# Performance work log

Measured on AMD Instinct MI355X. Metric: run time of the kernel, lower is better.

Reference implementation:

```python
import jax, jax.numpy as jnp
import numpy as np

N_NODES = 50000
LN_EPS = 1e-5


def gcn_conv(x, src, dst, norm, W, b):
    # PyG GCNConv: h = x @ W, then symmetric-normalized scatter-add, then bias.
    h = x @ W                                   # [N, out]
    msg = h[src] * norm[:, None]                # [E+N, out] gathered, scaled
    out = jax.ops.segment_sum(msg, dst, num_segments=N_NODES)
    return out + b


def layer_norm(x, gamma, beta):
    mu = jnp.mean(x, axis=-1, keepdims=True)
    var = jnp.var(x, axis=-1, keepdims=True)
    return (x - mu) * jax.lax.rsqrt(var + LN_EPS) * gamma + beta


def setup_inputs() -> dict:
    key = jax.random.key(0)
    ks = jax.random.split(key, 8)
    N, E, D = N_NODES, 1600000, 128
    x = jax.random.normal(ks[0], (N, D), dtype=jnp.float32)
    edge_index = jax.random.randint(ks[1], (2, E), 0, N, dtype=jnp.int64)
    s = 1.0 / np.sqrt(D)
    return {
        "x": x,
        "edge_index": edge_index,
        "W1": jax.random.uniform(ks[2], (D, D), jnp.float32, -s, s),
        "b1": jnp.zeros((D,), jnp.float32),
        "g1": jnp.ones((D,), jnp.float32),
        "be1": jnp.zeros((D,), jnp.float32),
        "W2": jax.random.uniform(ks[3], (D, D), jnp.float32, -s, s),
        "b2": jnp.zeros((D,), jnp.float32),
        "g2": jnp.ones((D,), jnp.float32),
        "be2": jnp.zeros((D,), jnp.float32),
    }


def reference(x, edge_index, W1, b1, g1, be1, W2, b2, g2, be2):
    # Add self-loops (PyG GCNConv default add_self_loops=True)
    sl = jnp.arange(N_NODES, dtype=edge_index.dtype)
    src = jnp.concatenate([edge_index[0], sl])
    dst = jnp.concatenate([edge_index[1], sl])
    # Symmetric normalization: deg^{-1/2}[src] * deg^{-1/2}[dst]
    deg = jax.ops.segment_sum(jnp.ones_like(src, dtype=x.dtype), dst,
                              num_segments=N_NODES)
    dinv = jnp.where(deg > 0, jax.lax.rsqrt(deg), 0.0)
    norm = dinv[src] * dinv[dst]

    h = gcn_conv(x, src, dst, norm, W1, b1)
    h = jax.nn.elu(layer_norm(h, g1, be1))
    h = gcn_conv(h, src, dst, norm, W2, b2)
    h = jax.nn.elu(layer_norm(h, g2, be2))
    return h
```

## Files before the change

### kernel.cpp

```cpp
#include <hip/hip_runtime.h>
#include <hip/hip_bf16.h>
#include <math.h>

#define N_NODES 50000
#define D 128
#define LN_EPS 1e-5f
#define NB 391
#define CHUNK 4096
#define GB 782
#define HB 512

typedef unsigned int u32;
typedef unsigned short u16;
typedef __attribute__((ext_vector_type(8))) short bf16x8;
typedef __attribute__((ext_vector_type(8))) unsigned short u16x8;
typedef __attribute__((ext_vector_type(4))) float f32x4;

static __device__ __forceinline__ u16 f2bf(float f) {
    union { float f; unsigned u; } v; v.f = f;
    unsigned r = v.u + 0x7fff + ((v.u >> 16) & 1);
    return (u16)(r >> 16);
}
static __device__ __forceinline__ float bf2f(u16 b) {
    union { unsigned u; float f; } v; v.u = ((unsigned)b) << 16;
    return v.f;
}
static __device__ __forceinline__ bf16x8 packf8(const float* p) {
    float4 f0 = *(const float4*)p;
    float4 f1 = *(const float4*)(p + 4);
    bf16x8 r;
    r[0] = (short)f2bf(f0.x); r[1] = (short)f2bf(f0.y);
    r[2] = (short)f2bf(f0.z); r[3] = (short)f2bf(f0.w);
    r[4] = (short)f2bf(f1.x); r[5] = (short)f2bf(f1.y);
    r[6] = (short)f2bf(f1.z); r[7] = (short)f2bf(f1.w);
    return r;
}

static __device__ __forceinline__ void agg_core8(
        const u16* __restrict__ H, const u16* __restrict__ csr_src,
        const float* __restrict__ dinv, int s, int cnt, int c0, float dn,
        float* __restrict__ a) {
    float b[8];
#pragma unroll
    for (int i = 0; i < 8; ++i) { a[i] = 0.f; b[i] = 0.f; }
    const u16* cp = csr_src + s;
    int j = 0;
    for (; j + 8 <= cnt; j += 8) {
        u32 i0 = cp[j],     i1 = cp[j + 1], i2 = cp[j + 2], i3 = cp[j + 3];
        u32 i4 = cp[j + 4], i5 = cp[j + 5], i6 = cp[j + 6], i7 = cp[j + 7];
        u16x8 g0 = *(const u16x8*)&H[(size_t)i0 * D + c0];
        u16x8 g1 = *(const u16x8*)&H[(size_t)i1 * D + c0];
        u16x8 g2 = *(const u16x8*)&H[(size_t)i2 * D + c0];
        u16x8 g3 = *(const u16x8*)&H[(size_t)i3 * D + c0];
        u16x8 g4 = *(const u16x8*)&H[(size_t)i4 * D + c0];
        u16x8 g5 = *(const u16x8*)&H[(size_t)i5 * D + c0];
        u16x8 g6 = *(const u16x8*)&H[(size_t)i6 * D + c0];
        u16x8 g7 = *(const u16x8*)&H[(size_t)i7 * D + c0];
        float w0 = dinv[i0] * dn, w1 = dinv[i1] * dn;
        float w2 = dinv[i2] * dn, w3 = dinv[i3] * dn;
        float w4 = dinv[i4] * dn, w5 = dinv[i5] * dn;
        float w6 = dinv[i6] * dn, w7 = dinv[i7] * dn;
#pragma unroll
        for (int i = 0; i < 8; ++i) {
            a[i] = fmaf(w0, bf2f(g0[i]), a[i]);
            b[i] = fmaf(w1, bf2f(g1[i]), b[i]);
            a[i] = fmaf(w2, bf2f(g2[i]), a[i]);
            b[i] = fmaf(w3, bf2f(g3[i]), b[i]);
            a[i] = fmaf(w4, bf2f(g4[i]), a[i]);
            b[i] = fmaf(w5, bf2f(g5[i]), b[i]);
            a[i] = fmaf(w6, bf2f(g6[i]), a[i]);
            b[i] = fmaf(w7, bf2f(g7[i]), b[i]);
        }
    }
    for (; j < cnt; ++j) {
        u32 i0 = cp[j];
        u16x8 g0 = *(const u16x8*)&H[(size_t)i0 * D + c0];
        float w0 = dinv[i0] * dn;
#pragma unroll
        for (int i = 0; i < 8; ++i) a[i] = fmaf(w0, bf2f(g0[i]), a[i]);
    }
#pragma unroll
    for (int i = 0; i < 8; ++i) a[i] += b[i];
}

static __device__ __forceinline__ void ln_elu8(
        float* __restrict__ a, int c0,
        const float* __restrict__ bias, const float* __restrict__ gamma,
        const float* __restrict__ beta) {
    float4 bv0 = *(const float4*)&bias[c0];
    float4 bv1 = *(const float4*)&bias[c0 + 4];
    a[0] += bv0.x; a[1] += bv0.y; a[2] += bv0.z; a[3] += bv0.w;
    a[4] += bv1.x; a[5] += bv1.y; a[6] += bv1.z; a[7] += bv1.w;
    float sum = 0.f, sq = 0.f;
#pragma unroll
    for (int i = 0; i < 8; ++i) { sum += a[i]; sq = fmaf(a[i], a[i], sq); }
#pragma unroll
    for (int m = 8; m > 0; m >>= 1) {
        sum += __shfl_xor(sum, m, 64);
        sq  += __shfl_xor(sq,  m, 64);
    }
    float mean = sum * (1.f / 128.f);
    float var  = sq * (1.f / 128.f) - mean * mean;
    float rstd = rsqrtf(var + LN_EPS);
    float4 gv0 = *(const float4*)&gamma[c0];
    float4 gv1 = *(const float4*)&gamma[c0 + 4];
    float4 ev0 = *(const float4*)&beta[c0];
    float4 ev1 = *(const float4*)&beta[c0 + 4];
    float gg[8] = {gv0.x, gv0.y, gv0.z, gv0.w, gv1.x, gv1.y, gv1.z, gv1.w};
    float ee[8] = {ev0.x, ev0.y, ev0.z, ev0.w, ev1.x, ev1.y, ev1.z, ev1.w};
#pragma unroll
    for (int i = 0; i < 8; ++i) {
        float y = (a[i] - mean) * rstd * gg[i] + ee[i];
        a[i] = y > 0.f ? y : expm1f(y);
    }
}

__global__ __launch_bounds__(256) void transpose_w(const float* __restrict__ W1,
                                                   const float* __restrict__ W2,
                                                   u16* __restrict__ W1T,
                                                   u16* __restrict__ W2T) {
    const float* w = (blockIdx.x == 0) ? W1 : W2;
    u16* wt = (blockIdx.x == 0) ? W1T : W2T;
    for (int idx = threadIdx.x; idx < D * D; idx += 256)
        wt[(idx & 127) * D + (idx >> 7)] = f2bf(w[idx]);
}

__global__ __launch_bounds__(256) void gemm1_hist(const float* __restrict__ X,
                                                  const u16* __restrict__ W1T,
                                                  u16* __restrict__ H,
                                                  const int* __restrict__ dstA,
                                                  u32* __restrict__ bucketCount, int E) {
    __shared__ u32 hist[NB];

    if (blockIdx.x >= GB) {
        for (int b = threadIdx.x; b < NB; b += 256) hist[b] = 0;
        __syncthreads();
        int stride = HB * 256;
        for (int e = (blockIdx.x - GB) * 256 + threadIdx.x; e < E; e += stride)
            atomicAdd(&hist[((u32)dstA[e]) >> 7], 1u);
        __syncthreads();
        for (int b = threadIdx.x; b < NB; b += 256)
            if (hist[b]) atomicAdd(&bucketCount[b], hist[b]);
        return;
    }
    int lane = threadIdx.x & 63;
    int wid  = threadIdx.x >> 6;
    int r    = lane & 15;
    int kg   = lane >> 4;

    for (int rb = blockIdx.x * 4 + wid; rb < N_NODES / 16; rb += GB * 4) {
        int row0 = rb * 16;
        const float* xp = X + (size_t)(row0 + r) * D + kg * 8;
        bf16x8 a0 = packf8(xp);      bf16x8 a1 = packf8(xp + 32);
        bf16x8 a2 = packf8(xp + 64); bf16x8 a3 = packf8(xp + 96);
#pragma unroll
        for (int tile = 0; tile < 8; ++tile) {
            const u16* wp = W1T + (size_t)(tile * 16 + r) * D + kg * 8;
            f32x4 acc = {0.f, 0.f, 0.f, 0.f};
            acc = __builtin_amdgcn_mfma_f32_16x16x32_bf16(a0, *(const bf16x8*)(wp),      acc, 0, 0, 0);
            acc = __builtin_amdgcn_mfma_f32_16x16x32_bf16(a1, *(const bf16x8*)(wp + 32), acc, 0, 0, 0);
            acc = __builtin_amdgcn_mfma_f32_16x16x32_bf16(a2, *(const bf16x8*)(wp + 64), acc, 0, 0, 0);
            acc = __builtin_amdgcn_mfma_f32_16x16x32_bf16(a3, *(const bf16x8*)(wp + 96), acc, 0, 0, 0);
#pragma unroll
            for (int i = 0; i < 4; ++i)
                H[(size_t)(row0 + kg * 4 + i) * D + tile * 16 + r] = f2bf(acc[i]);
        }
    }
}

__global__ __launch_bounds__(512) void partition_kernel(const int* __restrict__ srcA,
                                                        const int* __restrict__ dstA,
                                                        const u32* __restrict__ bucketCount,
                                                        u32* __restrict__ relCursor,
                                                        u32* __restrict__ ebuf, int E) {
    __shared__ u32 sc[512];
    __shared__ u32 ebS[NB], cntA[NB], cntB[NB], base[NB];
    int t = threadIdx.x;
    u32 bc = (t < NB) ? bucketCount[t] : 0u;
    sc[t] = bc;
    for (int b = t; b < NB; b += 512) { cntA[b] = 0; cntB[b] = 0; }
    __syncthreads();
    for (int off = 1; off < 512; off <<= 1) {
        u32 v = sc[t] + ((t >= off) ? sc[t - off] : 0u);
        __syncthreads();
        sc[t] = v;
        __syncthreads();
    }
    if (t < NB) ebS[t] = sc[t] - bc;
    __syncthreads();

    int e0 = blockIdx.x * CHUNK;
    int e1 = min(e0 + CHUNK, E);
    for (int e = e0 + t; e < e1; e += 512)
        atomicAdd(&cntA[((u32)dstA[e]) >> 7], 1u);
    __syncthreads();
    for (int b = t; b < NB; b += 512)
        if (cntA[b]) base[b] = ebS[b] + atomicAdd(&relCursor[b], cntA[b]);
    __syncthreads();
    for (int e = e0 + t; e < e1; e += 512) {
        u32 d = (u32)dstA[e], sv = (u32)srcA[e];
        u32 b = d >> 7;
        u32 off = atomicAdd(&cntB[b], 1u);
        ebuf[base[b] + off] = (sv << 16) | d;
    }
}

__global__ __launch_bounds__(256) void bucket_build(const u32* __restrict__ ebuf,
                                                    const u32* __restrict__ bucketCount,
                                                    u16* __restrict__ csr_src,
                                                    int* __restrict__ startArr,
                                                    float* __restrict__ dinv) {
    int b = blockIdx.x, t = threadIdx.x;
    __shared__ u32 red[256];
    __shared__ u32 cnt[128], sc[128], cur[128];
    u32 partial = 0;
    for (int i = t; i < b; i += 256) partial += bucketCount[i];
    red[t] = partial;
    if (t < 128) cnt[t] = 0;
    __syncthreads();
    for (int off = 128; off > 0; off >>= 1) {
        if (t < off) red[t] += red[t + off];
        __syncthreads();
    }
    u32 eb0 = red[0];
    u32 eb1 = eb0 + bucketCount[b];
    u32 cs  = eb0 + 128u * (u32)b;

    int nodeBase = b << 7;
    int nNodes = min(128, N_NODES - nodeBase);
    for (u32 e = eb0 + t; e < eb1; e += 256)
        atomicAdd(&cnt[ebuf[e] & 127u], 1u);
    __syncthreads();
    u32 myCnt = 0;
    if (t < 128) {
        myCnt = (t < nNodes) ? cnt[t] + 1u : 0u;
        sc[t] = myCnt;
    }
    __syncthreads();
    for (int off = 1; off < 128; off <<= 1) {
        u32 v = 0;
        if (t < 128) v = sc[t] + ((t >= off) ? sc[t - off] : 0u);
        __syncthreads();
        if (t < 128) sc[t] = v;
        __syncthreads();
    }
    if (t < nNodes) {
        u32 excl = sc[t] - myCnt;
        int i = nodeBase + t;
        startArr[i] = (int)(cs + excl);
        dinv[i] = rsqrtf((float)myCnt);
        csr_src[cs + excl] = (u16)i;
        cur[t] = excl + 1u;
        if (b == NB - 1 && t == nNodes - 1)
            startArr[N_NODES] = (int)(cs + sc[t]);
    }
    __syncthreads();
    for (u32 e = eb0 + t; e < eb1; e += 256) {
        u32 p = ebuf[e];
        u32 pos = atomicAdd(&cur[p & 127u], 1u);
        csr_src[cs + pos] = (u16)(p >> 16);
    }
}

__global__ __launch_bounds__(256) void agg_gemm(
        const u16* __restrict__ H, const u16* __restrict__ csr_src,
        const int* __restrict__ startArr, const float* __restrict__ dinv,
        const float* __restrict__ bias, const float* __restrict__ gamma,
        const float* __restrict__ beta,
        const u16* __restrict__ W2T, u16* __restrict__ H2) {
    __shared__ __align__(16) u16 X2[16][136];

    int t = threadIdx.x;
    int grp = t >> 4;
    int l   = t & 15;
    int c0  = l * 8;
    int node = blockIdx.x * 16 + grp;
    int s   = startArr[node];
    int cnt = startArr[node + 1] - s;
    float dn = dinv[node];

    float a[8];
    agg_core8(H, csr_src, dinv, s, cnt, c0, dn, a);
    ln_elu8(a, c0, bias, gamma, beta);

    u16x8 o;
#pragma unroll
    for (int i = 0; i < 8; ++i) o[i] = f2bf(a[i]);
    *(u16x8*)&X2[grp][c0] = o;
    __syncthreads();

    int lane = t & 63;
    int wv   = t >> 6;
    int r    = lane & 15;
    int kg   = lane >> 4;
    int row0 = blockIdx.x * 16;

    const u16* xp = &X2[r][kg * 8];
    bf16x8 a0f = *(const bf16x8*)(xp);
    bf16x8 a1f = *(const bf16x8*)(xp + 32);
    bf16x8 a2f = *(const bf16x8*)(xp + 64);
    bf16x8 a3f = *(const bf16x8*)(xp + 96);
#pragma unroll
    for (int tile = wv; tile < 8; tile += 4) {
        const u16* wp = W2T + (size_t)(tile * 16 + r) * D + kg * 8;
        f32x4 acc = {0.f, 0.f, 0.f, 0.f};
        acc = __builtin_amdgcn_mfma_f32_16x16x32_bf16(a0f, *(const bf16x8*)(wp),      acc, 0, 0, 0);
        acc = __builtin_amdgcn_mfma_f32_16x16x32_bf16(a1f, *(const bf16x8*)(wp + 32), acc, 0, 0, 0);
        acc = __builtin_amdgcn_mfma_f32_16x16x32_bf16(a2f, *(const bf16x8*)(wp + 64), acc, 0, 0, 0);
        acc = __builtin_amdgcn_mfma_f32_16x16x32_bf16(a3f, *(const bf16x8*)(wp + 96), acc, 0, 0, 0);
#pragma unroll
        for (int i = 0; i < 4; ++i)
            H2[(size_t)(row0 + kg * 4 + i) * D + tile * 16 + r] = f2bf(acc[i]);
    }
}

__global__ __launch_bounds__(256) void agg_ln_elu(
        const u16* __restrict__ H, const u16* __restrict__ csr_src,
        const int* __restrict__ startArr, const float* __restrict__ dinv,
        const float* __restrict__ bias, const float* __restrict__ gamma,
        const float* __restrict__ beta, float* __restrict__ out) {
    int t = threadIdx.x;
    int node = blockIdx.x * 16 + (t >> 4);
    int l    = t & 15;
    int c0   = l * 8;
    int s    = startArr[node];
    int cnt  = startArr[node + 1] - s;
    float dn = dinv[node];

    float a[8];
    agg_core8(H, csr_src, dinv, s, cnt, c0, dn, a);
    ln_elu8(a, c0, bias, gamma, beta);

    f32x4 o0 = {a[0], a[1], a[2], a[3]};
    f32x4 o1 = {a[4], a[5], a[6], a[7]};
    float* op = out + (size_t)node * D + c0;
    __builtin_nontemporal_store(o0, (f32x4*)op);
    __builtin_nontemporal_store(o1, (f32x4*)(op + 4));
}

extern "C" void kernel_launch(void* const* d_in, const int* in_sizes, int n_in,
                              void* d_out, int out_size, void* d_ws, size_t ws_size,
                              hipStream_t stream) {
    const float* x   = (const float*)d_in[0];
    const int*  eidx = (const int*)d_in[1];
    const float* W1  = (const float*)d_in[2];
    const float* b1  = (const float*)d_in[3];
    const float* g1  = (const float*)d_in[4];
    const float* be1 = (const float*)d_in[5];
    const float* W2  = (const float*)d_in[6];
    const float* b2  = (const float*)d_in[7];
    const float* g2  = (const float*)d_in[8];
    const float* be2 = (const float*)d_in[9];

    int E = in_sizes[1] / 2;
    const int* srcA = eidx;
    const int* dstA = eidx + E;

    char* p = (char*)d_ws;
    auto alloc = [&](size_t bytes) {
        char* r = p;
        p += (bytes + 255) & ~(size_t)255;
        return r;
    };
    u32*   ctr      = (u32*)alloc((size_t)1024 * 4);
    u32*   ebuf     = (u32*)alloc((size_t)E * 4);
    u16*   csr_src  = (u16*)alloc((size_t)(E + N_NODES) * 2);
    int*   startArr = (int*)alloc((size_t)(N_NODES + 1) * 4);
    float* dinv     = (float*)alloc((size_t)N_NODES * 4);
    u16*   w1t      = (u16*)alloc((size_t)D * D * 2);
    u16*   w2t      = (u16*)alloc((size_t)D * D * 2);
    u16*   h        = (u16*)alloc((size_t)N_NODES * D * 2);
    u16*   h2       = (u16*)alloc((size_t)N_NODES * D * 2);
    float* outp     = (float*)d_out;

    u32* bucketCount = ctr;
    u32* relCursor   = ctr + 512;

    int pb = (E + CHUNK - 1) / CHUNK;
    int fb = N_NODES / 16;

    hipError_t e0 = hipMemsetAsync(ctr, 0, 1024 * 4, stream);
    (void)e0;
    transpose_w     <<<2, 256, 0, stream>>>(W1, W2, w1t, w2t);
    gemm1_hist      <<<GB + HB, 256, 0, stream>>>(x, w1t, h, dstA, bucketCount, E);
    partition_kernel<<<pb, 512, 0, stream>>>(srcA, dstA, bucketCount, relCursor, ebuf, E);
    bucket_build    <<<NB, 256, 0, stream>>>(ebuf, bucketCount, csr_src, startArr, dinv);
    agg_gemm        <<<fb, 256, 0, stream>>>(h, csr_src, startArr, dinv,
                                             b1, g1, be1, w2t, h2);
    agg_ln_elu      <<<fb, 256, 0, stream>>>(h2, csr_src, startArr, dinv,
                                             b2, g2, be2, outp);
}
```

Baseline: 295.1 us.

## Regroup kernels: fuse weight transpose with histogram, GEMM1 with partition

The weight transpose now runs as a tiled shared-memory transpose in 32 blocks beside the edge histogram, replacing the separate two-block transpose launch. The first GEMM moves out of the histogram kernel into the partition kernel, where extra blocks compute it alongside partitioning. This removes one launch and lets the serial two-block transpose run in parallel with the histogram. GEMM1 now runs with 512-thread blocks (8 waves per block), which may change occupancy and contend with partition work.

```diff
diff --git a/kernel.cpp b/kernel.cpp
--- a/kernel.cpp
+++ b/kernel.cpp
@@ -7,8 +7,10 @@
 #define LN_EPS 1e-5f
 #define NB 391
 #define CHUNK 4096
-#define GB 782
+#define TB 32
 #define HB 512
+#define PB 391
+#define GB2 391
 
 typedef unsigned int u32;
 typedef unsigned short u16;
@@ -115,40 +117,66 @@
     }
 }
 
-__global__ __launch_bounds__(256) void transpose_w(const float* __restrict__ W1,
-                                                   const float* __restrict__ W2,
-                                                   u16* __restrict__ W1T,
-                                                   u16* __restrict__ W2T) {
-    const float* w = (blockIdx.x == 0) ? W1 : W2;
-    u16* wt = (blockIdx.x == 0) ? W1T : W2T;
-    for (int idx = threadIdx.x; idx < D * D; idx += 256)
-        wt[(idx & 127) * D + (idx >> 7)] = f2bf(w[idx]);
-}
-
-__global__ __launch_bounds__(256) void gemm1_hist(const float* __restrict__ X,
-                                                  const u16* __restrict__ W1T,
-                                                  u16* __restrict__ H,
+__global__ __launch_bounds__(256) void trans_hist(const float* __restrict__ W1,
+                                                  const float* __restrict__ W2,
+                                                  u16* __restrict__ W1T,
+                                                  u16* __restrict__ W2T,
                                                   const int* __restrict__ dstA,
                                                   u32* __restrict__ bucketCount, int E) {
     __shared__ u32 hist[NB];
 
-    if (blockIdx.x >= GB) {
-        for (int b = threadIdx.x; b < NB; b += 256) hist[b] = 0;
-        __syncthreads();
-        int stride = HB * 256;
-        for (int e = (blockIdx.x - GB) * 256 + threadIdx.x; e < E; e += stride)
-            atomicAdd(&hist[((u32)dstA[e]) >> 7], 1u);
-        __syncthreads();
-        for (int b = threadIdx.x; b < NB; b += 256)
-            if (hist[b]) atomicAdd(&bucketCount[b], hist[b]);
+    if (blockIdx.x < TB) {
+        __shared__ u16 tile[32][33];
+        int mat  = blockIdx.x >> 4;
+        int tl   = blockIdx.x & 15;
+        int bi   = (tl >> 2) * 32;
+        int bj   = (tl & 3) * 32;
+        const float* w = mat ? W2 : W1;
+        u16* wt = mat ? W2T : W1T;
+        int t = threadIdx.x;
+        int lr = t >> 5, lc = t & 31;
+#pragma unroll
+        for (int pass = 0; pass < 4; ++pass) {
+            int r = lr + pass * 8;
+            tile[r][lc] = f2bf(w[(size_t)(bi + r) * D + bj + lc]);
+        }
+        __syncthreads();
+#pragma unroll
+        for (int pass = 0; pass < 4; ++pass) {
+            int c = lr + pass * 8;
+            wt[(size_t)(bj + c) * D + bi + lc] = tile[lc][c];
+        }
         return;
     }
-    int lane = threadIdx.x & 63;
-    int wid  = threadIdx.x >> 6;
-    int r    = lane & 15;
-    int kg   = lane >> 4;
-
-    for (int rb = blockIdx.x * 4 + wid; rb < N_NODES / 16; rb += GB * 4) {
+    for (int b = threadIdx.x; b < NB; b += 256) hist[b] = 0;
+    __syncthreads();
+    int stride = HB * 256;
+    for (int e = (blockIdx.x - TB) * 256 + threadIdx.x; e < E; e += stride)
+        atomicAdd(&hist[((u32)dstA[e]) >> 7], 1u);
+    __syncthreads();
+    for (int b = threadIdx.x; b < NB; b += 256)
+        if (hist[b]) atomicAdd(&bucketCount[b], hist[b]);
+}
+
+__global__ __launch_bounds__(512) void part_gemm(const int* __restrict__ srcA,
+                                                 const int* __restrict__ dstA,
+                                                 const u32* __restrict__ bucketCount,
+                                                 u32* __restrict__ relCursor,
+                                                 u32* __restrict__ ebuf, int E,
+                                                 const float* __restrict__ X,
+                                                 const u16* __restrict__ W1T,
+                                                 u16* __restrict__ H) {
+    __shared__ u32 sc[512];
+    __shared__ u32 ebS[NB], cntA[NB], cntB[NB], base[NB];
+    int t = threadIdx.x;
+
+    if (blockIdx.x >= PB) {
+        int lane = t & 63;
+        int wid  = t >> 6;
+        int r    = lane & 15;
+        int kg   = lane >> 4;
+        int rb   = (blockIdx.x - PB) * 8 + wid;
+        if (rb >= N_NODES / 16) return;
         int row0 = rb * 16;
         const float* xp = X + (size_t)(row0 + r) * D + kg * 8;
         bf16x8 a0 = packf8(xp);      bf16x8 a1 = packf8(xp + 32);
@@ -165,17 +193,9 @@
             for (int i = 0; i < 4; ++i)
                 H[(size_t)(row0 + kg * 4 + i) * D + tile * 16 + r] = f2bf(acc[i]);
         }
-    }
-}
-
-__global__ __launch_bounds__(512) void partition_kernel(const int* __restrict__ srcA,
-                                                        const int* __restrict__ dstA,
-                                                        const u32* __restrict__ bucketCount,
-                                                        u32* __restrict__ relCursor,
-                                                        u32* __restrict__ ebuf, int E) {
-    __shared__ u32 sc[512];
-    __shared__ u32 ebS[NB], cntA[NB], cntB[NB], base[NB];
-    int t = threadIdx.x;
+        return;
+    }
+
     u32 bc = (t < NB) ? bucketCount[t] : 0u;
     sc[t] = bc;
     for (int b = t; b < NB; b += 512) { cntA[b] = 0; cntB[b] = 0; }
@@ -376,17 +396,16 @@
     u32* bucketCount = ctr;
     u32* relCursor   = ctr + 512;
 
-    int pb = (E + CHUNK - 1) / CHUNK;
     int fb = N_NODES / 16;
 
     hipError_t e0 = hipMemsetAsync(ctr, 0, 1024 * 4, stream);
     (void)e0;
-    transpose_w     <<<2, 256, 0, stream>>>(W1, W2, w1t, w2t);
-    gemm1_hist      <<<GB + HB, 256, 0, stream>>>(x, w1t, h, dstA, bucketCount, E);
-    partition_kernel<<<pb, 512, 0, stream>>>(srcA, dstA, bucketCount, relCursor, ebuf, E);
-    bucket_build    <<<NB, 256, 0, stream>>>(ebuf, bucketCount, csr_src, startArr, dinv);
-    agg_gemm        <<<fb, 256, 0, stream>>>(h, csr_src, startArr, dinv,
-                                             b1, g1, be1, w2t, h2);
-    agg_ln_elu      <<<fb, 256, 0, stream>>>(h2, csr_src, startArr, dinv,
-                                             b2, g2, be2, outp);
-}
+    trans_hist  <<<TB + HB, 256, 0, stream>>>(W1, W2, w1t, w2t, dstA, bucketCount, E);
+    part_gemm   <<<PB + GB2, 512, 0, stream>>>(srcA, dstA, bucketCount, relCursor,
+                                               ebuf, E, x, w1t, h);
+    bucket_build<<<NB, 256, 0, stream>>>(ebuf, bucketCount, csr_src, startArr, dinv);
+    agg_gemm    <<<fb, 256, 0, stream>>>(h, csr_src, startArr, dinv,
+                                         b1, g1, be1, w2t, h2);
+    agg_ln_elu  <<<fb, 256, 0, stream>>>(h2, csr_src, startArr, dinv,
+                                         b2, g2, be2, outp);
+}
```

Result: faster. 278.9 us (-5.5%).

## Fuse weight transpose into gemm1_hist and stage W1 in shared memory

Applied to the files above, without the earlier changes.

Removes the separate two-block transpose_w launch. Each GEMM block now converts and transposes W1 into a padded LDS tile, and 16 extra blocks transpose W2 with a 32x32 shared tile. This removes one serial kernel launch and the slow two-block transpose, and the GEMM reads B fragments from LDS instead of global memory. In exchange, each of the 782 GEMM blocks redoes the 16K-element W1 conversion, uses about 35KB of LDS (which may lower occupancy), and the padded LDS rows may cause bank conflicts on the bf16x8 reads.

```diff
diff --git a/kernel.cpp b/kernel.cpp
--- a/kernel.cpp
+++ b/kernel.cpp
@@ -9,6 +9,7 @@
 #define CHUNK 4096
 #define GB 782
 #define HB 512
+#define TB2 16
 
 typedef unsigned int u32;
 typedef unsigned short u16;
@@ -115,23 +116,36 @@
     }
 }
 
-__global__ __launch_bounds__(256) void transpose_w(const float* __restrict__ W1,
-                                                   const float* __restrict__ W2,
-                                                   u16* __restrict__ W1T,
-                                                   u16* __restrict__ W2T) {
-    const float* w = (blockIdx.x == 0) ? W1 : W2;
-    u16* wt = (blockIdx.x == 0) ? W1T : W2T;
-    for (int idx = threadIdx.x; idx < D * D; idx += 256)
-        wt[(idx & 127) * D + (idx >> 7)] = f2bf(w[idx]);
-}
-
 __global__ __launch_bounds__(256) void gemm1_hist(const float* __restrict__ X,
-                                                  const u16* __restrict__ W1T,
+                                                  const float* __restrict__ W1,
                                                   u16* __restrict__ H,
                                                   const int* __restrict__ dstA,
-                                                  u32* __restrict__ bucketCount, int E) {
+                                                  u32* __restrict__ bucketCount, int E,
+                                                  const float* __restrict__ W2,
+                                                  u16* __restrict__ W2T) {
+    __shared__ __align__(16) u16 WT[D][136];
     __shared__ u32 hist[NB];
-
+    __shared__ u16 tile[32][33];
+
+    if (blockIdx.x >= GB + HB) {
+        int tl = blockIdx.x - GB - HB;
+        int bi = (tl >> 2) * 32;
+        int bj = (tl & 3) * 32;
+        int t = threadIdx.x;
+        int lr = t >> 5, lc = t & 31;
+#pragma unroll
+        for (int pass = 0; pass < 4; ++pass) {
+            int r = lr + pass * 8;
+            tile[r][lc] = f2bf(W2[(size_t)(bi + r) * D + bj + lc]);
+        }
+        __syncthreads();
+#pragma unroll
+        for (int pass = 0; pass < 4; ++pass) {
+            int c = lr + pass * 8;
+            W2T[(size_t)(bj + c) * D + bi + lc] = tile[lc][c];
+        }
+        return;
+    }
     if (blockIdx.x >= GB) {
         for (int b = threadIdx.x; b < NB; b += 256) hist[b] = 0;
         __syncthreads();
@@ -143,6 +157,12 @@
             if (hist[b]) atomicAdd(&bucketCount[b], hist[b]);
         return;
     }
+    for (int idx = threadIdx.x; idx < D * D; idx += 256) {
+        int k = idx >> 7, c = idx & 127;
+        WT[c][k] = f2bf(W1[idx]);
+    }
+    __syncthreads();
+
     int lane = threadIdx.x & 63;
     int wid  = threadIdx.x >> 6;
     int r    = lane & 15;
@@ -154,8 +174,8 @@
         bf16x8 a0 = packf8(xp);      bf16x8 a1 = packf8(xp + 32);
         bf16x8 a2 = packf8(xp + 64); bf16x8 a3 = packf8(xp + 96);
 #pragma unroll
-        for (int tile = 0; tile < 8; ++tile) {
-            const u16* wp = W1T + (size_t)(tile * 16 + r) * D + kg * 8;
+        for (int t8 = 0; t8 < 8; ++t8) {
+            const u16* wp = &WT[t8 * 16 + r][kg * 8];
             f32x4 acc = {0.f, 0.f, 0.f, 0.f};
             acc = __builtin_amdgcn_mfma_f32_16x16x32_bf16(a0, *(const bf16x8*)(wp),      acc, 0, 0, 0);
             acc = __builtin_amdgcn_mfma_f32_16x16x32_bf16(a1, *(const bf16x8*)(wp + 32), acc, 0, 0, 0);
@@ -163,7 +183,7 @@
             acc = __builtin_amdgcn_mfma_f32_16x16x32_bf16(a3, *(const bf16x8*)(wp + 96), acc, 0, 0, 0);
 #pragma unroll
             for (int i = 0; i < 4; ++i)
-                H[(size_t)(row0 + kg * 4 + i) * D + tile * 16 + r] = f2bf(acc[i]);
+                H[(size_t)(row0 + kg * 4 + i) * D + t8 * 16 + r] = f2bf(acc[i]);
         }
     }
 }
@@ -367,7 +387,6 @@
     u16*   csr_src  = (u16*)alloc((size_t)(E + N_NODES) * 2);
     int*   startArr = (int*)alloc((size_t)(N_NODES + 1) * 4);
     float* dinv     = (float*)alloc((size_t)N_NODES * 4);
-    u16*   w1t      = (u16*)alloc((size_t)D * D * 2);
     u16*   w2t      = (u16*)alloc((size_t)D * D * 2);
     u16*   h        = (u16*)alloc((size_t)N_NODES * D * 2);
     u16*   h2       = (u16*)alloc((size_t)N_NODES * D * 2);
@@ -381,8 +400,8 @@
 
     hipError_t e0 = hipMemsetAsync(ctr, 0, 1024 * 4, stream);
     (void)e0;
-    transpose_w     <<<2, 256, 0, stream>>>(W1, W2, w1t, w2t);
-    gemm1_hist      <<<GB + HB, 256, 0, stream>>>(x, w1t, h, dstA, bucketCount, E);
+    gemm1_hist      <<<GB + HB + TB2, 256, 0, stream>>>(x, W1, h, dstA, bucketCount,
+                                                        E, W2, w2t);
     partition_kernel<<<pb, 512, 0, stream>>>(srcA, dstA, bucketCount, relCursor, ebuf, E);
     bucket_build    <<<NB, 256, 0, stream>>>(ebuf, bucketCount, csr_src, startArr, dinv);
     agg_gemm        <<<fb, 256, 0, stream>>>(h, csr_src, startArr, dinv,
```

After: 274.5 us. -7.0%, faster.
